# Kernel tuning notes

Measured on AMD Instinct MI355X. Metric: run time of the kernel, lower is better.

## Reference

```python
import jax, jax.numpy as jnp
import numpy as np

B, S, H = 2, 2048, 2048
NH, NKV = 16, 4
HD = H // NH          # 128
N_REP = NH // NKV     # 4


def _rotate_half(x):
    x1, x2 = x[..., : x.shape[-1] // 2], x[..., x.shape[-1] // 2 :]
    return jnp.concatenate((-x2, x1), axis=-1)


def setup_inputs() -> dict:
    key = jax.random.key(0)
    ks = jax.random.split(key, 5)
    hidden_states = jax.random.normal(ks[0], (B, S, H), dtype=jnp.float32)
    # true rotary tables [max_seq_len, head_dim]
    inv_freq = 1.0 / (10000.0 ** (np.arange(0, HD, 2, dtype=np.float32) / HD))
    t = np.arange(S, dtype=np.float32)
    freqs = np.outer(t, inv_freq)                    # [S, HD/2]
    emb = np.concatenate([freqs, freqs], axis=-1)    # [S, HD]
    cos = jnp.asarray(np.cos(emb))
    sin = jnp.asarray(np.sin(emb))
    Wq = jax.random.normal(ks[1], (H, NH * HD), dtype=jnp.float32) * 0.02
    Wk = jax.random.normal(ks[2], (H, NKV * HD), dtype=jnp.float32) * 0.02
    Wv = jax.random.normal(ks[3], (H, NKV * HD), dtype=jnp.float32) * 0.02
    Wo = jax.random.normal(ks[4], (NH * HD, H), dtype=jnp.float32) * 0.02
    attention_mask = jnp.ones((B, S), dtype=jnp.float32)  # 1 = keep
    return {"hidden_states": hidden_states, "cos": cos, "sin": sin,
            "Wq": Wq, "Wk": Wk, "Wv": Wv, "Wo": Wo,
            "attention_mask": attention_mask}


def reference(hidden_states, cos, sin, Wq, Wk, Wv, Wo, attention_mask):
    # Decoder self-attention: is_causal=True, use_rope=True, no cache, eval (dropout off).
    x = hidden_states
    b, s, _ = x.shape
    q = jnp.einsum('bsh,hd->bsd', x, Wq).reshape(b, s, NH, HD).transpose(0, 2, 1, 3)   # [b,nh,s,hd]
    k = jnp.einsum('bsh,hd->bsd', x, Wk).reshape(b, s, NKV, HD)
    v = jnp.einsum('bsh,hd->bsd', x, Wv).reshape(b, s, NKV, HD)
    # GQA repeat_kv: each kv head repeated n_rep times contiguously
    k = jnp.repeat(k, N_REP, axis=2).transpose(0, 2, 1, 3)   # [b,nh,s,hd]
    v = jnp.repeat(v, N_REP, axis=2).transpose(0, 2, 1, 3)
    # RoPE
    c = cos[:s][None, None, :, :]
    sn = sin[:s][None, None, :, :]
    q = q * c + _rotate_half(q) * sn
    k = k * c + _rotate_half(k) * sn
    # attention scores
    scores = jnp.einsum('bhqd,bhkd->bhqk', q, k) / jnp.sqrt(jnp.float32(HD))
    neg_inf = jnp.finfo(scores.dtype).min
    causal = jnp.triu(jnp.full((s, s), neg_inf, dtype=scores.dtype), k=1)
    scores = scores + causal[None, None, :, :]
    pad = (1.0 - attention_mask[:, None, None, :].astype(scores.dtype)) * neg_inf
    scores = scores + pad
    attn = jax.nn.softmax(scores.astype(jnp.float32), axis=-1).astype(q.dtype)
    out = jnp.einsum('bhqk,bhkd->bhqd', attn, v)             # [b,nh,s,hd]
    out = out.transpose(0, 2, 1, 3).reshape(b, s, NH * HD)
    return jnp.einsum('bsd,dh->bsh', out, Wo)
```

## Files before the change

### kernel.cpp

```cpp
#include <hip/hip_runtime.h>
#include <hip/hip_bf16.h>


typedef __bf16 bf16;
typedef __bf16 bf16x8 __attribute__((ext_vector_type(8)));
typedef __bf16 bf16x4 __attribute__((ext_vector_type(4)));
typedef float  f32x4  __attribute__((ext_vector_type(4)));

#define MFMA_BF16(a, b, c) __builtin_amdgcn_mfma_f32_16x16x32_bf16((a), (b), (c), 0, 0, 0)

__device__ __forceinline__ void glds16(const bf16* g, char* l) {
  __builtin_amdgcn_global_load_lds((__attribute__((address_space(1))) const void*)g,
                                   (__attribute__((address_space(3))) void*)l, 16, 0, 0);
}

__global__ __launch_bounds__(256) void k_cvt_bf16(const float* __restrict__ in,
                                                  bf16* __restrict__ out, int n4) {
  int i = blockIdx.x * 256 + threadIdx.x;
  if (i < n4) {
    float4 v = ((const float4*)in)[i];
    bf16x4 o;
    o[0] = (bf16)v.x; o[1] = (bf16)v.y; o[2] = (bf16)v.z; o[3] = (bf16)v.w;
    ((bf16x4*)out)[i] = o;
  }
}

__global__ __launch_bounds__(256) void k_transpose_w4(const float* __restrict__ Wq,
                                                      const float* __restrict__ Wk,
                                                      const float* __restrict__ Wv,
                                                      const float* __restrict__ Wo,
                                                      bf16* __restrict__ Wtq,
                                                      bf16* __restrict__ Wtk,
                                                      bf16* __restrict__ Wtv,
                                                      bf16* __restrict__ Wto) {
  int z = blockIdx.z;
  const float* W; bf16* Wt; int N;
  if (z == 0)      { W = Wq; Wt = Wtq; N = 2048; }
  else if (z == 1) { W = Wo; Wt = Wto; N = 2048; }
  else if (z == 2) { W = Wk; Wt = Wtk; N = 512; }
  else             { W = Wv; Wt = Wtv; N = 512; }
  int nb = blockIdx.y * 32;
  if (nb >= N) return;
  __shared__ float tile[32][33];
  int tx = threadIdx.x, ty = threadIdx.y;
  int kb = blockIdx.x * 32;
#pragma unroll
  for (int i = 0; i < 4; ++i)
    tile[ty + i * 8][tx] = W[(size_t)(kb + ty + i * 8) * N + nb + tx];
  __syncthreads();
#pragma unroll
  for (int i = 0; i < 4; ++i)
    Wt[(size_t)(nb + ty + i * 8) * 2048 + kb + tx] = (bf16)tile[tx][ty + i * 8];
}

__global__ __launch_bounds__(256) void k_transpose_v(const bf16* __restrict__ V,
                                                     bf16* __restrict__ Vt) {
  __shared__ bf16 tile[32][33];
  int tx = threadIdx.x, ty = threadIdx.y;
  int b = blockIdx.z;
  int sb = blockIdx.x * 32, cb = blockIdx.y * 32;
#pragma unroll
  for (int i = 0; i < 4; ++i)
    tile[ty + i * 8][tx] = V[(size_t)(b * 2048 + sb + ty + i * 8) * 512 + cb + tx];
  __syncthreads();
#pragma unroll
  for (int i = 0; i < 4; ++i)
    Vt[(size_t)(b * 512 + cb + ty + i * 8) * 2048 + sb + tx] = tile[tx][ty + i * 8];
}

template <typename OUT>
__device__ void gemm_block(const bf16* __restrict__ A, const bf16* __restrict__ Bt,
                           OUT* __restrict__ C, int K, int ldc,
                           int rbase, int cbase, char* sm,
                           float rope_scl, const float* __restrict__ cosb,
                           const float* __restrict__ sinb) {
  const int tid = threadIdx.x;
  const int lane = tid & 63, wid = tid >> 6;
  const int l15 = lane & 15, lg = lane >> 4;
  char* Asm = sm;
  char* Bsm = sm + 32768;

  f32x4 acc[2][8];
#pragma unroll
  for (int i = 0; i < 2; ++i)
#pragma unroll
    for (int j = 0; j < 8; ++j)
#pragma unroll
      for (int r = 0; r < 4; ++r) acc[i][j][r] = 0.0f;

  const int ob = wid * 4096 + lane * 16;
  auto stage = [&](int buf, int kb) {
#pragma unroll
    for (int c = 0; c < 4; ++c) {
      int o = ob + c * 1024;
      int r = o >> 7;
      int cc = ((o >> 4) & 7) ^ (r & 7);
      int dst = wid * 4096 + c * 1024 + buf * 16384;
      glds16(A + (size_t)(rbase + r) * K + kb + cc * 8, Asm + dst);
      glds16(Bt + (size_t)(cbase + r) * K + kb + cc * 8, Bsm + dst);
    }
  };

  stage(0, 0);
  __syncthreads();
  const int nk = K >> 6;
  for (int t = 0; t < nk; ++t) {
    if (t + 1 < nk) stage((t + 1) & 1, (t + 1) << 6);
    const char* At  = Asm + (t & 1) * 16384;
    const char* Bti = Bsm + (t & 1) * 16384;
#pragma unroll
    for (int ks = 0; ks < 2; ++ks) {
      bf16x8 a[2], b[8];
#pragma unroll
      for (int rf = 0; rf < 2; ++rf) {
        int r = wid * 32 + rf * 16 + l15;
        int slot = (ks * 4 + lg) ^ (r & 7);
        a[rf] = *(const bf16x8*)(At + r * 128 + slot * 16);
      }
#pragma unroll
      for (int nf = 0; nf < 8; ++nf) {
        int n = nf * 16 + l15;
        int slot = (ks * 4 + lg) ^ (n & 7);
        b[nf] = *(const bf16x8*)(Bti + n * 128 + slot * 16);
      }
#pragma unroll
      for (int rf = 0; rf < 2; ++rf)
#pragma unroll
        for (int nf = 0; nf < 8; ++nf)
          acc[rf][nf] = MFMA_BF16(a[rf], b[nf], acc[rf][nf]);
    }
    __syncthreads();
  }

  if (rope_scl != 0.0f) {
#pragma unroll
    for (int rf = 0; rf < 2; ++rf)
#pragma unroll
      for (int r = 0; r < 4; ++r) {
        int s = (rbase + wid * 32 + rf * 16 + lg * 4 + r) & 2047;
#pragma unroll
        for (int nf = 0; nf < 4; ++nf) {
          int d = nf * 16 + l15;
          float v0 = acc[rf][nf][r], v1 = acc[rf][nf + 4][r];
          float c0 = cosb[s * 128 + d],      c1 = cosb[s * 128 + d + 64];
          float s0 = sinb[s * 128 + d],      s1 = sinb[s * 128 + d + 64];
          acc[rf][nf][r]     = (v0 * c0 - v1 * s0) * rope_scl;
          acc[rf][nf + 4][r] = (v1 * c1 + v0 * s1) * rope_scl;
        }
      }
  }

#pragma unroll
  for (int rf = 0; rf < 2; ++rf)
#pragma unroll
    for (int nf = 0; nf < 8; ++nf)
#pragma unroll
      for (int r = 0; r < 4; ++r) {
        int row = rbase + wid * 32 + rf * 16 + lg * 4 + r;
        int col = cbase + nf * 16 + l15;
        C[(size_t)row * ldc + col] = (OUT)acc[rf][nf][r];
      }
}

__global__ __launch_bounds__(256, 2) void k_gemm_qkv(const bf16* __restrict__ X,
                                                     const bf16* __restrict__ Wtq,
                                                     const bf16* __restrict__ Wtk,
                                                     const bf16* __restrict__ Wtv,
                                                     bf16* __restrict__ Q,
                                                     bf16* __restrict__ Ko,
                                                     bf16* __restrict__ Vo,
                                                     const float* __restrict__ cosb,
                                                     const float* __restrict__ sinb,
                                                     float sclq) {
  __shared__ alignas(16) char sm[65536];
  int nb = blockIdx.y;
  int rbase = blockIdx.x * 128;
  const bf16* Bt; bf16* C; int ldc, cbase; float rs;
  if (nb < 16)      { Bt = Wtq; C = Q;  ldc = 2048; cbase = nb * 128;        rs = sclq; }
  else if (nb < 20) { Bt = Wtk; C = Ko; ldc = 512;  cbase = (nb - 16) * 128; rs = 1.0f; }
  else              { Bt = Wtv; C = Vo; ldc = 512;  cbase = (nb - 20) * 128; rs = 0.0f; }
  gemm_block<bf16>(X, Bt, C, 2048, ldc, rbase, cbase, sm, rs, cosb, sinb);
}

__global__ __launch_bounds__(256, 2) void k_gemm_o(const bf16* __restrict__ AO,
                                                   const bf16* __restrict__ Wto,
                                                   float* __restrict__ Out) {
  __shared__ alignas(16) char sm[65536];
  gemm_block<float>(AO, Wto, Out, 2048, 2048, blockIdx.x * 128, blockIdx.y * 128, sm,
                    0.0f, nullptr, nullptr);
}

__global__ __launch_bounds__(256, 4) void k_fattn(const bf16* __restrict__ Qg,
                                                  const bf16* __restrict__ Kg,
                                                  const bf16* __restrict__ Vtg,
                                                  bf16* __restrict__ AO) {
  __shared__ alignas(16) char sm[37888];
  const int lane = threadIdx.x & 63, wid = threadIdx.x >> 6;
  const int l15 = lane & 15, lg = lane >> 4;
  const int wg = blockIdx.x;
  const int grp = wg & 7;
  const int b = grp >> 2, kv = grp & 3;
  const int inner = wg >> 3;
  const int h = kv * 4 + (inner & 3);
  const int si = inner >> 2;
  const int strip = (si & 1) ? (si >> 1) : (31 - (si >> 1));
  const int q0 = strip * 64 + wid * 16;
  const int nt = 2 * (strip + 1);
  char* Pw = sm + 32768 + wid * 1280;

  bf16x8 qf[4];
#pragma unroll
  for (int kf = 0; kf < 4; ++kf)
    qf[kf] = *(const bf16x8*)(Qg + (size_t)(b * 2048 + q0 + l15) * 2048 + h * 128 + kf * 32 + lg * 8);

  f32x4 o[8];
#pragma unroll
  for (int j = 0; j < 8; ++j)
#pragma unroll
    for (int r = 0; r < 4; ++r) o[j][r] = 0.0f;
  float mrun = -3e38f, lrun = 0.0f;

  const bf16* ksrc[2];
  const bf16* vsrc[2];
  int kdst[2], vdst[2];
#pragma unroll
  for (int j = 0; j < 2; ++j) {
    int c = wid * 128 + j * 64 + lane;
    int kr = c >> 4, kslot = c & 15;
    int kcc = kslot ^ (kr & 15);
    ksrc[j] = Kg + (size_t)(b * 2048 + kr) * 512 + kv * 128 + kcc * 8;
    kdst[j] = wid * 2048 + j * 1024;
    int vr = c >> 2, vslot = c & 3;
    int vcc = vslot ^ ((vr >> 1) & 3);
    vsrc[j] = Vtg + (size_t)((b * 4 + kv) * 128 + vr) * 2048 + vcc * 8;
    vdst[j] = 16384 + wid * 2048 + j * 1024;
  }
  auto stageKV = [&](int buf) {
#pragma unroll
    for (int j = 0; j < 2; ++j) {
      glds16(ksrc[j], sm + buf * 8192 + kdst[j]);
      glds16(vsrc[j], sm + buf * 8192 + vdst[j]);
      ksrc[j] += 32 * 512;
      vsrc[j] += 32;
    }
  };

  stageKV(0);
  __syncthreads();

  for (int t = 0; t < nt; ++t) {
    const int kb = t << 5;
    if (t + 1 < nt) stageKV((t + 1) & 1);
    const char* Kt = sm + (t & 1) * 8192;
    const char* Vt = sm + 16384 + (t & 1) * 8192;

    f32x4 sa[2];
#pragma unroll
    for (int j = 0; j < 2; ++j)
#pragma unroll
      for (int r = 0; r < 4; ++r) sa[j][r] = 0.0f;
#pragma unroll
    for (int kf = 0; kf < 4; ++kf) {
#pragma unroll
      for (int nf = 0; nf < 2; ++nf) {
        int slot = (kf * 4 + lg) ^ l15;
        bf16x8 bk = *(const bf16x8*)(Kt + (nf * 16 + l15) * 256 + slot * 16);
        sa[nf] = MFMA_BF16(bk, qf[kf], sa[nf]);
      }
    }

    if (kb + 31 > q0) {
      const int qi = q0 + l15;
#pragma unroll
      for (int nf = 0; nf < 2; ++nf)
#pragma unroll
        for (int r = 0; r < 4; ++r)
          if (kb + nf * 16 + lg * 4 + r > qi) sa[nf][r] = -3e38f;
    }

    float mx = sa[0][0];
#pragma unroll
    for (int nf = 0; nf < 2; ++nf)
#pragma unroll
      for (int r = 0; r < 4; ++r) mx = fmaxf(mx, sa[nf][r]);
    mx = fmaxf(mx, __shfl_xor(mx, 16));
    mx = fmaxf(mx, __shfl_xor(mx, 32));
    if (!__all(mx - mrun <= 8.0f)) {
      float mnew = fmaxf(mrun, mx);
      float fac = __builtin_amdgcn_exp2f(mrun - mnew);
      lrun *= fac;
      f32x4 fv;
#pragma unroll
      for (int r = 0; r < 4; ++r) fv[r] = __shfl(fac, lg * 4 + r);
#pragma unroll
      for (int j = 0; j < 8; ++j) o[j] *= fv;
      mrun = mnew;
    }
    float rs = 0.0f;
#pragma unroll
    for (int nf = 0; nf < 2; ++nf) {
      bf16x4 pk;
#pragma unroll
      for (int r = 0; r < 4; ++r) {
        float p = __builtin_amdgcn_exp2f(sa[nf][r] - mrun);
        rs += p;
        pk[r] = (bf16)p;
      }
      *(bf16x4*)(Pw + l15 * 80 + nf * 32 + lg * 8) = pk;
    }
    rs += __shfl_xor(rs, 16);
    rs += __shfl_xor(rs, 32);
    lrun += rs;

    bf16x8 pa = *(const bf16x8*)(Pw + l15 * 80 + lg * 16);
#pragma unroll
    for (int nf2 = 0; nf2 < 8; ++nf2) {
      int d = nf2 * 16 + l15;
      int slot = lg ^ ((d >> 1) & 3);
      bf16x8 vb = *(const bf16x8*)(Vt + d * 64 + slot * 16);
      o[nf2] = MFMA_BF16(pa, vb, o[nf2]);
    }
    __syncthreads();
  }

  f32x4 linv;
#pragma unroll
  for (int r = 0; r < 4; ++r) linv[r] = 1.0f / __shfl(lrun, lg * 4 + r);
#pragma unroll
  for (int j = 0; j < 8; ++j)
#pragma unroll
    for (int r = 0; r < 4; ++r) {
      size_t row = (size_t)(b * 2048 + q0 + lg * 4 + r);
      AO[row * 2048 + h * 128 + j * 16 + l15] = (bf16)(o[j][r] * linv[r]);
    }
}

extern "C" void kernel_launch(void* const* d_in, const int* in_sizes, int n_in,
                              void* d_out, int out_size, void* d_ws, size_t ws_size,
                              hipStream_t stream) {
  const float* hs   = (const float*)d_in[0];
  const float* cosb = (const float*)d_in[1];
  const float* sinb = (const float*)d_in[2];
  const float* Wq   = (const float*)d_in[3];
  const float* Wk   = (const float*)d_in[4];
  const float* Wv   = (const float*)d_in[5];
  const float* Wo   = (const float*)d_in[6];
  float* Out = (float*)d_out;

  char* ws = (char*)d_ws;
  size_t off = 0;
  auto alloc = [&](size_t bytes) { char* p = ws + off; off += bytes; return p; };
  bf16* Xbf = (bf16*)alloc((size_t)4096 * 2048 * 2);
  bf16* Wtq = (bf16*)alloc((size_t)2048 * 2048 * 2);
  bf16* Wtk = (bf16*)alloc((size_t)512 * 2048 * 2);
  bf16* Wtv = (bf16*)alloc((size_t)512 * 2048 * 2);
  bf16* Wto = (bf16*)alloc((size_t)2048 * 2048 * 2);
  bf16* Qb  = (bf16*)alloc((size_t)4096 * 2048 * 2);
  bf16* Kb  = (bf16*)alloc((size_t)4096 * 512 * 2);
  bf16* Vb  = (bf16*)alloc((size_t)4096 * 512 * 2);
  bf16* Vtb = (bf16*)alloc((size_t)4096 * 512 * 2);
  bf16* AO  = (bf16*)alloc((size_t)4096 * 2048 * 2);

  const float SCLQ = 0.08838834764831845f * 1.4426950408889634f;

  dim3 tb(32, 8);
  k_cvt_bf16<<<8192, 256, 0, stream>>>(hs, Xbf, 2097152);
  k_transpose_w4<<<dim3(64, 64, 4), tb, 0, stream>>>(Wq, Wk, Wv, Wo, Wtq, Wtk, Wtv, Wto);
  k_gemm_qkv<<<dim3(32, 24), 256, 0, stream>>>(Xbf, Wtq, Wtk, Wtv, Qb, Kb, Vb,
                                               cosb, sinb, SCLQ);
  k_transpose_v<<<dim3(64, 16, 2), tb, 0, stream>>>(Vb, Vtb);
  k_fattn<<<1024, 256, 0, stream>>>(Qb, Kb, Vtb, AO);
  k_gemm_o<<<dim3(32, 16), 256, 0, stream>>>(AO, Wto, Out);
}
```

Baseline: 202.6 us.

## Fuse V transpose into QKV GEMM epilogue, reorder attention strips, add MFMA priority

```diff
diff --git a/kernel.cpp b/kernel.cpp
--- a/kernel.cpp
+++ b/kernel.cpp
@@ -53,27 +53,13 @@
     Wt[(size_t)(nb + ty + i * 8) * 2048 + kb + tx] = (bf16)tile[tx][ty + i * 8];
 }
 
-__global__ __launch_bounds__(256) void k_transpose_v(const bf16* __restrict__ V,
-                                                     bf16* __restrict__ Vt) {
-  __shared__ bf16 tile[32][33];
-  int tx = threadIdx.x, ty = threadIdx.y;
-  int b = blockIdx.z;
-  int sb = blockIdx.x * 32, cb = blockIdx.y * 32;
-#pragma unroll
-  for (int i = 0; i < 4; ++i)
-    tile[ty + i * 8][tx] = V[(size_t)(b * 2048 + sb + ty + i * 8) * 512 + cb + tx];
-  __syncthreads();
-#pragma unroll
-  for (int i = 0; i < 4; ++i)
-    Vt[(size_t)(b * 512 + cb + ty + i * 8) * 2048 + sb + tx] = tile[tx][ty + i * 8];
-}
-
 template <typename OUT>
 __device__ void gemm_block(const bf16* __restrict__ A, const bf16* __restrict__ Bt,
                            OUT* __restrict__ C, int K, int ldc,
                            int rbase, int cbase, char* sm,
                            float rope_scl, const float* __restrict__ cosb,
-                           const float* __restrict__ sinb) {
+                           const float* __restrict__ sinb,
+                           bf16* __restrict__ vtr, int vkv) {
   const int tid = threadIdx.x;
   const int lane = tid & 63, wid = tid >> 6;
   const int l15 = lane & 15, lg = lane >> 4;
@@ -150,6 +136,31 @@
       }
   }
 
+  if (vtr != nullptr) {
+#pragma unroll
+    for (int rf = 0; rf < 2; ++rf)
+#pragma unroll
+      for (int nf = 0; nf < 8; ++nf) {
+        int s0 = wid * 32 + rf * 16 + lg * 4;
+        int d = nf * 16 + l15;
+        bf16x4 pk;
+#pragma unroll
+        for (int r = 0; r < 4; ++r) pk[r] = (bf16)acc[rf][nf][r];
+        *(bf16x4*)(sm + d * 256 + ((s0 * 2) ^ ((d & 15) << 4))) = pk;
+      }
+    __syncthreads();
+    const int b4 = (rbase >> 11) * 4;
+    const int scol = rbase & 2047;
+    const int so = tid & 15;
+#pragma unroll
+    for (int i = 0; i < 8; ++i) {
+      int d = (tid >> 4) + i * 16;
+      bf16x8 v = *(const bf16x8*)(sm + d * 256 + ((so * 16) ^ ((d & 15) << 4)));
+      *(bf16x8*)(vtr + (size_t)((b4 + vkv) * 128 + d) * 2048 + scol + so * 8) = v;
+    }
+    return;
+  }
+
 #pragma unroll
   for (int rf = 0; rf < 2; ++rf)
 #pragma unroll
@@ -168,18 +179,23 @@
                                                      const bf16* __restrict__ Wtv,
                                                      bf16* __restrict__ Q,
                                                      bf16* __restrict__ Ko,
-                                                     bf16* __restrict__ Vo,
+                                                     bf16* __restrict__ Vt,
                                                      const float* __restrict__ cosb,
                                                      const float* __restrict__ sinb,
                                                      float sclq) {
   __shared__ alignas(16) char sm[65536];
   int nb = blockIdx.y;
   int rbase = blockIdx.x * 128;
-  const bf16* Bt; bf16* C; int ldc, cbase; float rs;
-  if (nb < 16)      { Bt = Wtq; C = Q;  ldc = 2048; cbase = nb * 128;        rs = sclq; }
-  else if (nb < 20) { Bt = Wtk; C = Ko; ldc = 512;  cbase = (nb - 16) * 128; rs = 1.0f; }
-  else              { Bt = Wtv; C = Vo; ldc = 512;  cbase = (nb - 20) * 128; rs = 0.0f; }
-  gemm_block<bf16>(X, Bt, C, 2048, ldc, rbase, cbase, sm, rs, cosb, sinb);
+  if (nb < 16) {
+    gemm_block<bf16>(X, Wtq, Q, 2048, 2048, rbase, nb * 128, sm, sclq, cosb, sinb,
+                     nullptr, 0);
+  } else if (nb < 20) {
+    gemm_block<bf16>(X, Wtk, Ko, 2048, 512, rbase, (nb - 16) * 128, sm, 1.0f, cosb, sinb,
+                     nullptr, 0);
+  } else {
+    gemm_block<bf16>(X, Wtv, (bf16*)nullptr, 2048, 512, rbase, (nb - 20) * 128, sm,
+                     0.0f, nullptr, nullptr, Vt, nb - 20);
+  }
 }
 
 __global__ __launch_bounds__(256, 2) void k_gemm_o(const bf16* __restrict__ AO,
@@ -187,7 +203,7 @@
                                                    float* __restrict__ Out) {
   __shared__ alignas(16) char sm[65536];
   gemm_block<float>(AO, Wto, Out, 2048, 2048, blockIdx.x * 128, blockIdx.y * 128, sm,
-                    0.0f, nullptr, nullptr);
+                    0.0f, nullptr, nullptr, nullptr, 0);
 }
 
 __global__ __launch_bounds__(256, 4) void k_fattn(const bf16* __restrict__ Qg,
@@ -202,8 +218,7 @@
   const int b = grp >> 2, kv = grp & 3;
   const int inner = wg >> 3;
   const int h = kv * 4 + (inner & 3);
-  const int si = inner >> 2;
-  const int strip = (si & 1) ? (si >> 1) : (31 - (si >> 1));
+  const int strip = 31 - (inner >> 2);
   const int q0 = strip * 64 + wid * 16;
   const int nt = 2 * (strip + 1);
   char* Pw = sm + 32768 + wid * 1280;
@@ -259,6 +274,7 @@
     for (int j = 0; j < 2; ++j)
 #pragma unroll
       for (int r = 0; r < 4; ++r) sa[j][r] = 0.0f;
+    __builtin_amdgcn_s_setprio(1);
 #pragma unroll
     for (int kf = 0; kf < 4; ++kf) {
 #pragma unroll
@@ -268,6 +284,7 @@
         sa[nf] = MFMA_BF16(bk, qf[kf], sa[nf]);
       }
     }
+    __builtin_amdgcn_s_setprio(0);
 
     if (kb + 31 > q0) {
       const int qi = q0 + l15;
@@ -313,6 +330,7 @@
     lrun += rs;
 
     bf16x8 pa = *(const bf16x8*)(Pw + l15 * 80 + lg * 16);
+    __builtin_amdgcn_s_setprio(1);
 #pragma unroll
     for (int nf2 = 0; nf2 < 8; ++nf2) {
       int d = nf2 * 16 + l15;
@@ -320,6 +338,7 @@
       bf16x8 vb = *(const bf16x8*)(Vt + d * 64 + slot * 16);
       o[nf2] = MFMA_BF16(pa, vb, o[nf2]);
     }
+    __builtin_amdgcn_s_setprio(0);
     __syncthreads();
   }
 
@@ -357,7 +376,6 @@
   bf16* Wto = (bf16*)alloc((size_t)2048 * 2048 * 2);
   bf16* Qb  = (bf16*)alloc((size_t)4096 * 2048 * 2);
   bf16* Kb  = (bf16*)alloc((size_t)4096 * 512 * 2);
-  bf16* Vb  = (bf16*)alloc((size_t)4096 * 512 * 2);
   bf16* Vtb = (bf16*)alloc((size_t)4096 * 512 * 2);
   bf16* AO  = (bf16*)alloc((size_t)4096 * 2048 * 2);
 
@@ -366,9 +384,8 @@
   dim3 tb(32, 8);
   k_cvt_bf16<<<8192, 256, 0, stream>>>(hs, Xbf, 2097152);
   k_transpose_w4<<<dim3(64, 64, 4), tb, 0, stream>>>(Wq, Wk, Wv, Wo, Wtq, Wtk, Wtv, Wto);
-  k_gemm_qkv<<<dim3(32, 24), 256, 0, stream>>>(Xbf, Wtq, Wtk, Wtv, Qb, Kb, Vb,
+  k_gemm_qkv<<<dim3(32, 24), 256, 0, stream>>>(Xbf, Wtq, Wtk, Wtv, Qb, Kb, Vtb,
                                                cosb, sinb, SCLQ);
-  k_transpose_v<<<dim3(64, 16, 2), tb, 0, stream>>>(Vb, Vtb);
   k_fattn<<<1024, 256, 0, stream>>>(Qb, Kb, Vtb, AO);
   k_gemm_o<<<dim3(32, 16), 256, 0, stream>>>(AO, Wto, Out);
 }
```

After: 202.1 us. Within noise of the previous version (-0.2%).
